# Kernel optimization log

Measured on AMD Instinct MI355X. Metric: run time of the kernel, lower is better.

Reference implementation:

```python
import jax, jax.numpy as jnp
import numpy as np

B, T, L, S, H = 128, 256, 64, 25, 128


def setup_inputs() -> dict:
    key = jax.random.key(0)
    ks = jax.random.split(key, 10)
    return {
        "k": jax.random.normal(ks[0], (B, T, L), jnp.float32),
        "K": jax.random.uniform(ks[1], (B, T, L), jnp.float32),  # positive precision increments
        "noise": jax.random.normal(ks[2], (T, S, B, L), jnp.float32),
        "log_Q": jax.random.normal(ks[3], (L,), jnp.float32),
        "m_0": jax.random.normal(ks[4], (L,), jnp.float32),
        "log_Q_0": jax.random.normal(ks[5], (L,), jnp.float32),
        "W1": jax.random.normal(ks[6], (L, H), jnp.float32) * 0.05,
        "b1": jax.random.normal(ks[7], (H,), jnp.float32) * 0.05,
        "W2": jax.random.normal(ks[8], (H, L), jnp.float32) * 0.05,
        "b2": jax.random.normal(ks[9], (L,), jnp.float32) * 0.05,
    }


def reference(k, K, noise, log_Q, m_0, log_Q_0, W1, b1, W2, b2):
    Q_diag = jax.nn.softplus(log_Q)            # [L]
    P_0 = jax.nn.softplus(log_Q_0)             # [L]

    def mean_fn(z):                            # residual tanh MLP dynamics, [..., L] -> [..., L]
        return z + jnp.tanh(z @ W1 + b1) @ W2 + b2

    # ---- t = 0 (filter_step_0) ----
    J_0 = 1.0 / P_0
    h_0 = J_0 * m_0
    J_f0 = J_0 + K[:, 0]                       # [B, L]
    P_f0 = 1.0 / J_f0
    m_f0 = P_f0 * (h_0 + k[:, 0])
    z_0 = m_f0 + jnp.sqrt(P_f0) * noise[0]     # [S, B, L]
    m_p0 = jnp.broadcast_to(m_0, (B, L))
    P_p0 = jnp.broadcast_to(P_0, (B, L))

    # ---- t >= 1 (predict_step_t + filter_step_t), diagonal of the moment-matched cov ----
    def step(z_prev, inputs):
        k_t, K_t, w_t = inputs                 # [B,L], [B,L], [S,B,L]
        m_th = mean_fn(z_prev)                 # [S, B, L]
        m_p = m_th.mean(axis=0)                # [B, L]
        # diag(P_p) = Q_diag + E[m^2] - m_p^2  (diagonal of -2*M_p - outer(m_p, m_p))
        P_p = Q_diag + (m_th * m_th).mean(axis=0) - m_p * m_p
        J_p = 1.0 / P_p
        J_f = J_p + K_t
        P_f = 1.0 / J_f
        m_f = P_f * (J_p * m_p + k_t)
        z_t = m_f + jnp.sqrt(P_f) * w_t        # [S, B, L]
        return z_t, (z_t, m_f, m_p, P_f, P_p)

    xs = (jnp.swapaxes(k[:, 1:], 0, 1), jnp.swapaxes(K[:, 1:], 0, 1), noise[1:])
    _, (z_rest, m_f_rest, m_p_rest, P_f_rest, P_p_rest) = jax.lax.scan(step, z_0, xs)

    z_f = jnp.moveaxis(jnp.concatenate([z_0[None], z_rest], axis=0), 0, 2)  # [S, B, T, L]
    stk = lambda a0, ar: jnp.swapaxes(jnp.concatenate([a0[None], ar], axis=0), 0, 1)  # [B, T, L]
    m_f = stk(m_f0, m_f_rest)
    m_p = stk(m_p0, m_p_rest)
    P_f = stk(P_f0, P_f_rest)
    P_p = stk(P_p0, P_p_rest)
    return z_f, m_f, m_p, P_f, P_p
```

## Files before the change

kernel.cpp:

```cpp
#include <hip/hip_runtime.h>
#include <math.h>


namespace {
constexpr int B = 128;
constexpr int T = 256;
constexpr int L = 64;
constexpr int S = 25;
constexpr int H = 128;
constexpr int NT = 256;
constexpr int LP = 72;
constexpr int HP = 136;

typedef __bf16 bf16x8 __attribute__((ext_vector_type(8)));
typedef __bf16 bf16x4 __attribute__((ext_vector_type(4)));
typedef float floatx4 __attribute__((ext_vector_type(4)));

__device__ __forceinline__ float softplus_f(float x) {
    return fmaxf(x, 0.0f) + log1pf(expf(-fabsf(x)));
}

__device__ __forceinline__ float tanh_fast(float x) {
    const float e = __builtin_amdgcn_exp2f(x * 2.885390081777927f);
    return 1.0f - 2.0f * __builtin_amdgcn_rcpf(e + 1.0f);
}

__device__ __forceinline__ void split4(const float v[4], bf16x4* h, bf16x4* l) {
    #pragma unroll
    for (int r = 0; r < 4; ++r) {
        const __bf16 hi = (__bf16)v[r];
        (*h)[r] = hi;
        (*l)[r] = (__bf16)(v[r] - (float)hi);
    }
}
}

__global__ __launch_bounds__(NT, 1)
void nlf_kernel(const float* __restrict__ kk,
                const float* __restrict__ KK,
                const float* __restrict__ noise,
                const float* __restrict__ log_Q,
                const float* __restrict__ m_0,
                const float* __restrict__ log_Q_0,
                const float* __restrict__ W1,
                const float* __restrict__ b1,
                const float* __restrict__ W2,
                const float* __restrict__ b2,
                float* __restrict__ out)
{
    const int b    = blockIdx.x;
    const int tid  = threadIdx.x;
    const int w    = tid >> 6;
    const int lane = tid & 63;
    const int r16  = lane & 15;
    const int q    = lane >> 4;
    const int lc   = w * 16 + q * 4;

    __shared__ __align__(16) __bf16 sW1h[H][LP];
    __shared__ __align__(16) __bf16 sW1l[H][LP];
    __shared__ __align__(16) __bf16 sW2h[L][HP];
    __shared__ __align__(16) __bf16 sW2l[L][HP];
    __shared__ __align__(16) __bf16 sThh[32][HP];
    __shared__ __align__(16) __bf16 sThl[32][HP];
    __shared__ __align__(16) __bf16 sZh[32][LP];
    __shared__ __align__(16) __bf16 sZl[32][LP];

    for (int i = tid; i < L * H; i += NT) {
        const int l = i >> 7, j = i & 127;
        const float v = W1[i];
        const __bf16 hi = (__bf16)v;
        sW1h[j][l] = hi;
        sW1l[j][l] = (__bf16)(v - (float)hi);
    }
    for (int i = tid; i < H * L; i += NT) {
        const int j = i >> 6, l2 = i & 63;
        const float v = W2[i];
        const __bf16 hi = (__bf16)v;
        sW2h[l2][j] = hi;
        sW2l[l2][j] = (__bf16)(v - (float)hi);
    }
    for (int i = tid; i < 7 * LP; i += NT) {
        sZh[25 + i / LP][i % LP] = (__bf16)0.0f;
        sZl[25 + i / LP][i % LP] = (__bf16)0.0f;
    }

    const float4 b2v = *(const float4*)&b2[lc];
    float4 b1v[2];
    b1v[0] = *(const float4*)&b1[(2 * w    ) * 16 + q * 4];
    b1v[1] = *(const float4*)&b1[(2 * w + 1) * 16 + q * 4];
    float qd4[4];
    #pragma unroll
    for (int r = 0; r < 4; ++r) qd4[r] = softplus_f(log_Q[lc + r]);

    float* out_zf = out;
    float* out_mf = out + (size_t)S * B * T * L;
    float* out_mp = out_mf + (size_t)B * T * L;
    float* out_Pf = out_mp + (size_t)B * T * L;
    float* out_Pp = out_Pf + (size_t)B * T * L;

    const bool m1ok = (r16 < S - 16);

    float zreg0[4];
    float zreg1[4] = {0.f, 0.f, 0.f, 0.f};

    {
        const float4 lq0 = *(const float4*)&log_Q_0[lc];
        const float4 m0v = *(const float4*)&m_0[lc];
        const float4 K0  = *(const float4*)&KK[((size_t)b * T + 0) * L + lc];
        const float4 k0  = *(const float4*)&kk[((size_t)b * T + 0) * L + lc];
        float mfv[4], spv[4];
        float4 mf4, pf4, pp4;
        #pragma unroll
        for (int r = 0; r < 4; ++r) {
            const float P0 = softplus_f((&lq0.x)[r]);
            const float J0 = 1.0f / P0;
            const float Jf = J0 + (&K0.x)[r];
            const float Pf = 1.0f / Jf;
            const float mf = Pf * (J0 * (&m0v.x)[r] + (&k0.x)[r]);
            mfv[r] = mf;
            spv[r] = sqrtf(Pf);
            (&mf4.x)[r] = mf; (&pf4.x)[r] = Pf; (&pp4.x)[r] = P0;
        }
        if (r16 == 0) {
            const size_t o = ((size_t)b * T + 0) * L + lc;
            *(float4*)&out_mf[o] = mf4;
            *(float4*)&out_mp[o] = m0v;
            *(float4*)&out_Pf[o] = pf4;
            *(float4*)&out_Pp[o] = pp4;
        }
        {
            const float4 nv = *(const float4*)&noise[(((size_t)0 * S + r16) * B + b) * L + lc];
            float zv[4];
            #pragma unroll
            for (int r = 0; r < 4; ++r) { zv[r] = fmaf(spv[r], (&nv.x)[r], mfv[r]); zreg0[r] = zv[r]; }
            bf16x4 h, l; split4(zv, &h, &l);
            *(bf16x4*)&sZh[r16][lc] = h;
            *(bf16x4*)&sZl[r16][lc] = l;
            *(float4*)&out_zf[(((size_t)r16 * B + b) * T + 0) * L + lc] = make_float4(zv[0], zv[1], zv[2], zv[3]);
        }
        if (m1ok) {
            const int s = 16 + r16;
            const float4 nv = *(const float4*)&noise[(((size_t)0 * S + s) * B + b) * L + lc];
            float zv[4];
            #pragma unroll
            for (int r = 0; r < 4; ++r) { zv[r] = fmaf(spv[r], (&nv.x)[r], mfv[r]); zreg1[r] = zv[r]; }
            bf16x4 h, l; split4(zv, &h, &l);
            *(bf16x4*)&sZh[s][lc] = h;
            *(bf16x4*)&sZl[s][lc] = l;
            *(float4*)&out_zf[(((size_t)s * B + b) * T + 0) * L + lc] = make_float4(zv[0], zv[1], zv[2], zv[3]);
        }
    }

    for (int t = 1; t < T; ++t) {
        const size_t bt = (size_t)b * T + t;
        const float4 kv = *(const float4*)&kk[bt * L + lc];
        const float4 Kv = *(const float4*)&KK[bt * L + lc];
        const float4 nv0 = *(const float4*)&noise[(((size_t)t * S + r16) * B + b) * L + lc];
        float4 nv1 = make_float4(0.f, 0.f, 0.f, 0.f);
        if (m1ok) nv1 = *(const float4*)&noise[(((size_t)t * S + 16 + r16) * B + b) * L + lc];

        __syncthreads();

        bf16x8 z0h[2], z0l[2], z1h[2], z1l[2];
        #pragma unroll
        for (int kb = 0; kb < 2; ++kb) {
            z0h[kb] = *(const bf16x8*)&sZh[r16][kb * 32 + q * 8];
            z0l[kb] = *(const bf16x8*)&sZl[r16][kb * 32 + q * 8];
            z1h[kb] = *(const bf16x8*)&sZh[16 + r16][kb * 32 + q * 8];
            z1l[kb] = *(const bf16x8*)&sZl[16 + r16][kb * 32 + q * 8];
        }
        #pragma unroll
        for (int tt = 0; tt < 2; ++tt) {
            const int jt = 2 * w + tt;
            floatx4 c0 = {0.f, 0.f, 0.f, 0.f};
            floatx4 c1 = {0.f, 0.f, 0.f, 0.f};
            #pragma unroll
            for (int kb = 0; kb < 2; ++kb) {
                const bf16x8 wh = *(const bf16x8*)&sW1h[jt * 16 + r16][kb * 32 + q * 8];
                const bf16x8 wl = *(const bf16x8*)&sW1l[jt * 16 + r16][kb * 32 + q * 8];
                c0 = __builtin_amdgcn_mfma_f32_16x16x32_bf16(wh, z0h[kb], c0, 0, 0, 0);
                c0 = __builtin_amdgcn_mfma_f32_16x16x32_bf16(wl, z0h[kb], c0, 0, 0, 0);
                c0 = __builtin_amdgcn_mfma_f32_16x16x32_bf16(wh, z0l[kb], c0, 0, 0, 0);
                c1 = __builtin_amdgcn_mfma_f32_16x16x32_bf16(wh, z1h[kb], c1, 0, 0, 0);
                c1 = __builtin_amdgcn_mfma_f32_16x16x32_bf16(wl, z1h[kb], c1, 0, 0, 0);
                c1 = __builtin_amdgcn_mfma_f32_16x16x32_bf16(wh, z1l[kb], c1, 0, 0, 0);
            }
            float tv[4];
            bf16x4 h, l;
            #pragma unroll
            for (int r = 0; r < 4; ++r) tv[r] = tanh_fast(c0[r] + (&b1v[tt].x)[r]);
            split4(tv, &h, &l);
            *(bf16x4*)&sThh[r16][jt * 16 + q * 4] = h;
            *(bf16x4*)&sThl[r16][jt * 16 + q * 4] = l;
            #pragma unroll
            for (int r = 0; r < 4; ++r) tv[r] = tanh_fast(c1[r] + (&b1v[tt].x)[r]);
            split4(tv, &h, &l);
            *(bf16x4*)&sThh[16 + r16][jt * 16 + q * 4] = h;
            *(bf16x4*)&sThl[16 + r16][jt * 16 + q * 4] = l;
        }
        __syncthreads();

        floatx4 d0 = {0.f, 0.f, 0.f, 0.f};
        floatx4 d1 = {0.f, 0.f, 0.f, 0.f};
        #pragma unroll
        for (int kb = 0; kb < 4; ++kb) {
            const bf16x8 ah  = *(const bf16x8*)&sW2h[w * 16 + r16][kb * 32 + q * 8];
            const bf16x8 al  = *(const bf16x8*)&sW2l[w * 16 + r16][kb * 32 + q * 8];
            const bf16x8 t0h = *(const bf16x8*)&sThh[r16][kb * 32 + q * 8];
            const bf16x8 t0l = *(const bf16x8*)&sThl[r16][kb * 32 + q * 8];
            const bf16x8 t1h = *(const bf16x8*)&sThh[16 + r16][kb * 32 + q * 8];
            const bf16x8 t1l = *(const bf16x8*)&sThl[16 + r16][kb * 32 + q * 8];
            d0 = __builtin_amdgcn_mfma_f32_16x16x32_bf16(ah, t0h, d0, 0, 0, 0);
            d0 = __builtin_amdgcn_mfma_f32_16x16x32_bf16(al, t0h, d0, 0, 0, 0);
            d0 = __builtin_amdgcn_mfma_f32_16x16x32_bf16(ah, t0l, d0, 0, 0, 0);
            d1 = __builtin_amdgcn_mfma_f32_16x16x32_bf16(ah, t1h, d1, 0, 0, 0);
            d1 = __builtin_amdgcn_mfma_f32_16x16x32_bf16(al, t1h, d1, 0, 0, 0);
            d1 = __builtin_amdgcn_mfma_f32_16x16x32_bf16(ah, t1l, d1, 0, 0, 0);
        }

        float sm[4], sq[4];
        #pragma unroll
        for (int r = 0; r < 4; ++r) {
            const float v0  = d0[r] + (&b2v.x)[r] + zreg0[r];
            const float v1  = d1[r] + (&b2v.x)[r] + zreg1[r];
            const float v1m = m1ok ? v1 : 0.0f;
            sm[r] = v0 + v1m;
            sq[r] = fmaf(v0, v0, v1m * v1m);
        }
        #pragma unroll
        for (int d = 1; d < 16; d <<= 1) {
            #pragma unroll
            for (int r = 0; r < 4; ++r) {
                sm[r] += __shfl_xor(sm[r], d);
                sq[r] += __shfl_xor(sq[r], d);
            }
        }

        float mfv[4], spv[4];
        float4 mf4, mp4, pf4, pp4;
        #pragma unroll
        for (int r = 0; r < 4; ++r) {
            const float mp  = sm[r] * (1.0f / S);
            const float msq = sq[r] * (1.0f / S);
            const float Pp  = qd4[r] + msq - mp * mp;
            const float Jp  = __builtin_amdgcn_rcpf(Pp);
            const float Jf  = Jp + (&Kv.x)[r];
            const float Pf  = __builtin_amdgcn_rcpf(Jf);
            const float mf  = Pf * fmaf(Jp, mp, (&kv.x)[r]);
            mfv[r] = mf;
            spv[r] = __builtin_amdgcn_sqrtf(Pf);
            (&mf4.x)[r] = mf; (&mp4.x)[r] = mp; (&pf4.x)[r] = Pf; (&pp4.x)[r] = Pp;
        }
        if (r16 == 0) {
            const size_t o = bt * L + lc;
            *(float4*)&out_mf[o] = mf4;
            *(float4*)&out_mp[o] = mp4;
            *(float4*)&out_Pf[o] = pf4;
            *(float4*)&out_Pp[o] = pp4;
        }

        {
            float zv[4];
            #pragma unroll
            for (int r = 0; r < 4; ++r) { zv[r] = fmaf(spv[r], (&nv0.x)[r], mfv[r]); zreg0[r] = zv[r]; }
            bf16x4 h, l; split4(zv, &h, &l);
            *(bf16x4*)&sZh[r16][lc] = h;
            *(bf16x4*)&sZl[r16][lc] = l;
            *(float4*)&out_zf[(((size_t)r16 * B + b) * T + t) * L + lc] = make_float4(zv[0], zv[1], zv[2], zv[3]);
        }
        if (m1ok) {
            const int s = 16 + r16;
            float zv[4];
            #pragma unroll
            for (int r = 0; r < 4; ++r) { zv[r] = fmaf(spv[r], (&nv1.x)[r], mfv[r]); zreg1[r] = zv[r]; }
            bf16x4 h, l; split4(zv, &h, &l);
            *(bf16x4*)&sZh[s][lc] = h;
            *(bf16x4*)&sZl[s][lc] = l;
            *(float4*)&out_zf[(((size_t)s * B + b) * T + t) * L + lc] = make_float4(zv[0], zv[1], zv[2], zv[3]);
        }
    }
}

extern "C" void kernel_launch(void* const* d_in, const int* in_sizes, int n_in,
                              void* d_out, int out_size, void* d_ws, size_t ws_size,
                              hipStream_t stream) {
    const float* kk      = (const float*)d_in[0];
    const float* KK      = (const float*)d_in[1];
    const float* noise   = (const float*)d_in[2];
    const float* log_Q   = (const float*)d_in[3];
    const float* m_0     = (const float*)d_in[4];
    const float* log_Q_0 = (const float*)d_in[5];
    const float* W1      = (const float*)d_in[6];
    const float* b1      = (const float*)d_in[7];
    const float* W2      = (const float*)d_in[8];
    const float* b2      = (const float*)d_in[9];
    float* outp          = (float*)d_out;

    nlf_kernel<<<dim3(B), dim3(NT), 0, stream>>>(
        kk, KK, noise, log_Q, m_0, log_Q_0, W1, b1, W2, b2, outp);
}
```

Measured before the change: 818.8 us.

## Keep MLP weights in registers, DPP reductions, lightweight barriers, pointer increments

```diff
diff --git a/kernel.cpp b/kernel.cpp
--- a/kernel.cpp
+++ b/kernel.cpp
@@ -32,6 +32,26 @@
         (*h)[r] = hi;
         (*l)[r] = (__bf16)(v[r] - (float)hi);
     }
+}
+
+template<int CTRL>
+__device__ __forceinline__ float dpp_radd(float x) {
+    const int yi = __builtin_amdgcn_update_dpp(
+        0, __builtin_bit_cast(int, x), CTRL, 0xf, 0xf, false);
+    return x + __builtin_bit_cast(float, yi);
+}
+__device__ __forceinline__ float reduce16(float x) {
+    x = dpp_radd<0x128>(x);
+    x = dpp_radd<0x124>(x);
+    x = dpp_radd<0x4E>(x);
+    x = dpp_radd<0xB1>(x);
+    return x;
+}
+
+__device__ __forceinline__ void lds_barrier() {
+    asm volatile("s_waitcnt lgkmcnt(0)" ::: "memory");
+    __builtin_amdgcn_s_barrier();
+    asm volatile("" ::: "memory");
 }
 }
 
@@ -83,6 +103,22 @@
         sZh[25 + i / LP][i % LP] = (__bf16)0.0f;
         sZl[25 + i / LP][i % LP] = (__bf16)0.0f;
     }
+    __syncthreads();
+
+    bf16x8 w1h[2][2], w1l[2][2];
+    #pragma unroll
+    for (int tt = 0; tt < 2; ++tt)
+        #pragma unroll
+        for (int kb = 0; kb < 2; ++kb) {
+            w1h[tt][kb] = *(const bf16x8*)&sW1h[(2 * w + tt) * 16 + r16][kb * 32 + q * 8];
+            w1l[tt][kb] = *(const bf16x8*)&sW1l[(2 * w + tt) * 16 + r16][kb * 32 + q * 8];
+        }
+    bf16x8 w2h[4], w2l[4];
+    #pragma unroll
+    for (int kb = 0; kb < 4; ++kb) {
+        w2h[kb] = *(const bf16x8*)&sW2h[w * 16 + r16][kb * 32 + q * 8];
+        w2l[kb] = *(const bf16x8*)&sW2l[w * 16 + r16][kb * 32 + q * 8];
+    }
 
     const float4 b2v = *(const float4*)&b2[lc];
     float4 b1v[2];
@@ -151,15 +187,25 @@
         }
     }
 
+    constexpr size_t DSEC  = (size_t)B * T * L;
+    constexpr size_t NSTEP = (size_t)S * B * L;
+    const float* pk  = kk    + ((size_t)b * T + 1) * L + lc;
+    const float* pK  = KK    + ((size_t)b * T + 1) * L + lc;
+    const float* pn0 = noise + (((size_t)1 * S + r16) * B + b) * L + lc;
+    const float* pn1 = noise + (((size_t)1 * S + 16 + r16) * B + b) * L + lc;
+    float* pz0 = out_zf + (((size_t)r16 * B + b) * T + 1) * L + lc;
+    float* pz1 = out_zf + (((size_t)(16 + r16) * B + b) * T + 1) * L + lc;
+    float* pmf = out_mf + ((size_t)b * T + 1) * L + lc;
+
     for (int t = 1; t < T; ++t) {
-        const size_t bt = (size_t)b * T + t;
-        const float4 kv = *(const float4*)&kk[bt * L + lc];
-        const float4 Kv = *(const float4*)&KK[bt * L + lc];
-        const float4 nv0 = *(const float4*)&noise[(((size_t)t * S + r16) * B + b) * L + lc];
+        const float4 kv  = *(const float4*)pk;
+        const float4 Kv  = *(const float4*)pK;
+        const float4 nv0 = *(const float4*)pn0;
         float4 nv1 = make_float4(0.f, 0.f, 0.f, 0.f);
-        if (m1ok) nv1 = *(const float4*)&noise[(((size_t)t * S + 16 + r16) * B + b) * L + lc];
-
-        __syncthreads();
+        if (m1ok) nv1 = *(const float4*)pn1;
+        pk += L; pK += L; pn0 += NSTEP; pn1 += NSTEP;
+
+        lds_barrier();
 
         bf16x8 z0h[2], z0l[2], z1h[2], z1l[2];
         #pragma unroll
@@ -171,20 +217,18 @@
         }
         #pragma unroll
         for (int tt = 0; tt < 2; ++tt) {
-            const int jt = 2 * w + tt;
             floatx4 c0 = {0.f, 0.f, 0.f, 0.f};
             floatx4 c1 = {0.f, 0.f, 0.f, 0.f};
             #pragma unroll
             for (int kb = 0; kb < 2; ++kb) {
-                const bf16x8 wh = *(const bf16x8*)&sW1h[jt * 16 + r16][kb * 32 + q * 8];
-                const bf16x8 wl = *(const bf16x8*)&sW1l[jt * 16 + r16][kb * 32 + q * 8];
-                c0 = __builtin_amdgcn_mfma_f32_16x16x32_bf16(wh, z0h[kb], c0, 0, 0, 0);
-                c0 = __builtin_amdgcn_mfma_f32_16x16x32_bf16(wl, z0h[kb], c0, 0, 0, 0);
-                c0 = __builtin_amdgcn_mfma_f32_16x16x32_bf16(wh, z0l[kb], c0, 0, 0, 0);
-                c1 = __builtin_amdgcn_mfma_f32_16x16x32_bf16(wh, z1h[kb], c1, 0, 0, 0);
-                c1 = __builtin_amdgcn_mfma_f32_16x16x32_bf16(wl, z1h[kb], c1, 0, 0, 0);
-                c1 = __builtin_amdgcn_mfma_f32_16x16x32_bf16(wh, z1l[kb], c1, 0, 0, 0);
+                c0 = __builtin_amdgcn_mfma_f32_16x16x32_bf16(w1h[tt][kb], z0h[kb], c0, 0, 0, 0);
+                c0 = __builtin_amdgcn_mfma_f32_16x16x32_bf16(w1l[tt][kb], z0h[kb], c0, 0, 0, 0);
+                c0 = __builtin_amdgcn_mfma_f32_16x16x32_bf16(w1h[tt][kb], z0l[kb], c0, 0, 0, 0);
+                c1 = __builtin_amdgcn_mfma_f32_16x16x32_bf16(w1h[tt][kb], z1h[kb], c1, 0, 0, 0);
+                c1 = __builtin_amdgcn_mfma_f32_16x16x32_bf16(w1l[tt][kb], z1h[kb], c1, 0, 0, 0);
+                c1 = __builtin_amdgcn_mfma_f32_16x16x32_bf16(w1h[tt][kb], z1l[kb], c1, 0, 0, 0);
             }
+            const int jt = 2 * w + tt;
             float tv[4];
             bf16x4 h, l;
             #pragma unroll
@@ -198,24 +242,22 @@
             *(bf16x4*)&sThh[16 + r16][jt * 16 + q * 4] = h;
             *(bf16x4*)&sThl[16 + r16][jt * 16 + q * 4] = l;
         }
-        __syncthreads();
+        lds_barrier();
 
         floatx4 d0 = {0.f, 0.f, 0.f, 0.f};
         floatx4 d1 = {0.f, 0.f, 0.f, 0.f};
         #pragma unroll
         for (int kb = 0; kb < 4; ++kb) {
-            const bf16x8 ah  = *(const bf16x8*)&sW2h[w * 16 + r16][kb * 32 + q * 8];
-            const bf16x8 al  = *(const bf16x8*)&sW2l[w * 16 + r16][kb * 32 + q * 8];
             const bf16x8 t0h = *(const bf16x8*)&sThh[r16][kb * 32 + q * 8];
             const bf16x8 t0l = *(const bf16x8*)&sThl[r16][kb * 32 + q * 8];
             const bf16x8 t1h = *(const bf16x8*)&sThh[16 + r16][kb * 32 + q * 8];
             const bf16x8 t1l = *(const bf16x8*)&sThl[16 + r16][kb * 32 + q * 8];
-            d0 = __builtin_amdgcn_mfma_f32_16x16x32_bf16(ah, t0h, d0, 0, 0, 0);
-            d0 = __builtin_amdgcn_mfma_f32_16x16x32_bf16(al, t0h, d0, 0, 0, 0);
-            d0 = __builtin_amdgcn_mfma_f32_16x16x32_bf16(ah, t0l, d0, 0, 0, 0);
-            d1 = __builtin_amdgcn_mfma_f32_16x16x32_bf16(ah, t1h, d1, 0, 0, 0);
-            d1 = __builtin_amdgcn_mfma_f32_16x16x32_bf16(al, t1h, d1, 0, 0, 0);
-            d1 = __builtin_amdgcn_mfma_f32_16x16x32_bf16(ah, t1l, d1, 0, 0, 0);
+            d0 = __builtin_amdgcn_mfma_f32_16x16x32_bf16(w2h[kb], t0h, d0, 0, 0, 0);
+            d0 = __builtin_amdgcn_mfma_f32_16x16x32_bf16(w2l[kb], t0h, d0, 0, 0, 0);
+            d0 = __builtin_amdgcn_mfma_f32_16x16x32_bf16(w2h[kb], t0l, d0, 0, 0, 0);
+            d1 = __builtin_amdgcn_mfma_f32_16x16x32_bf16(w2h[kb], t1h, d1, 0, 0, 0);
+            d1 = __builtin_amdgcn_mfma_f32_16x16x32_bf16(w2l[kb], t1h, d1, 0, 0, 0);
+            d1 = __builtin_amdgcn_mfma_f32_16x16x32_bf16(w2h[kb], t1l, d1, 0, 0, 0);
         }
 
         float sm[4], sq[4];
@@ -224,16 +266,8 @@
             const float v0  = d0[r] + (&b2v.x)[r] + zreg0[r];
             const float v1  = d1[r] + (&b2v.x)[r] + zreg1[r];
             const float v1m = m1ok ? v1 : 0.0f;
-            sm[r] = v0 + v1m;
-            sq[r] = fmaf(v0, v0, v1m * v1m);
-        }
-        #pragma unroll
-        for (int d = 1; d < 16; d <<= 1) {
-            #pragma unroll
-            for (int r = 0; r < 4; ++r) {
-                sm[r] += __shfl_xor(sm[r], d);
-                sq[r] += __shfl_xor(sq[r], d);
-            }
+            sm[r] = reduce16(v0 + v1m);
+            sq[r] = reduce16(fmaf(v0, v0, v1m * v1m));
         }
 
         float mfv[4], spv[4];
@@ -252,12 +286,12 @@
             (&mf4.x)[r] = mf; (&mp4.x)[r] = mp; (&pf4.x)[r] = Pf; (&pp4.x)[r] = Pp;
         }
         if (r16 == 0) {
-            const size_t o = bt * L + lc;
-            *(float4*)&out_mf[o] = mf4;
-            *(float4*)&out_mp[o] = mp4;
-            *(float4*)&out_Pf[o] = pf4;
-            *(float4*)&out_Pp[o] = pp4;
-        }
+            *(float4*)pmf             = mf4;
+            *(float4*)(pmf + DSEC)    = mp4;
+            *(float4*)(pmf + 2*DSEC)  = pf4;
+            *(float4*)(pmf + 3*DSEC)  = pp4;
+        }
+        pmf += L;
 
         {
             float zv[4];
@@ -266,18 +300,18 @@
             bf16x4 h, l; split4(zv, &h, &l);
             *(bf16x4*)&sZh[r16][lc] = h;
             *(bf16x4*)&sZl[r16][lc] = l;
-            *(float4*)&out_zf[(((size_t)r16 * B + b) * T + t) * L + lc] = make_float4(zv[0], zv[1], zv[2], zv[3]);
+            *(float4*)pz0 = make_float4(zv[0], zv[1], zv[2], zv[3]);
         }
         if (m1ok) {
-            const int s = 16 + r16;
             float zv[4];
             #pragma unroll
             for (int r = 0; r < 4; ++r) { zv[r] = fmaf(spv[r], (&nv1.x)[r], mfv[r]); zreg1[r] = zv[r]; }
             bf16x4 h, l; split4(zv, &h, &l);
-            *(bf16x4*)&sZh[s][lc] = h;
-            *(bf16x4*)&sZl[s][lc] = l;
-            *(float4*)&out_zf[(((size_t)s * B + b) * T + t) * L + lc] = make_float4(zv[0], zv[1], zv[2], zv[3]);
-        }
+            *(bf16x4*)&sZh[16 + r16][lc] = h;
+            *(bf16x4*)&sZl[16 + r16][lc] = l;
+            *(float4*)pz1 = make_float4(zv[0], zv[1], zv[2], zv[3]);
+        }
+        pz0 += L; pz1 += L;
     }
 }
 
```

Result: faster. 717.4 us (-12.4%).
